# Kernel optimization log

Hardware: AMD Instinct MI355X
Metric: run time of the kernel (lower is better)

## Reference

```python
import jax, jax.numpy as jnp
import numpy as np

N_NODES = 100000
N_EDGES = 1600000
D_IN = 64
D_OUT = 64
NEG_SLOPE = 0.2


def setup_inputs() -> dict:
    key = jax.random.key(0)
    ks = jax.random.split(key, 10)
    x = jax.random.normal(ks[0], (N_NODES, D_IN), dtype=jnp.float32)
    edge_index = jax.random.randint(ks[1], (2, N_EDGES), 0, N_NODES, dtype=jnp.int64)
    # glorot-ish scales
    s_lin = 1.0 / np.sqrt(D_IN)
    W_lin = jax.random.normal(ks[2], (D_IN, D_OUT), dtype=jnp.float32) * s_lin
    att_src = jax.random.normal(ks[3], (D_OUT,), dtype=jnp.float32) * s_lin
    att_dst = jax.random.normal(ks[4], (D_OUT,), dtype=jnp.float32) * s_lin
    bias = jnp.zeros((D_OUT,), dtype=jnp.float32)
    W1 = jax.random.normal(ks[5], (D_IN, D_OUT // 2), dtype=jnp.float32) * s_lin
    b1 = jnp.zeros((D_OUT // 2,), dtype=jnp.float32)
    W2 = jax.random.normal(ks[6], (D_OUT // 2, 1), dtype=jnp.float32) * (1.0 / np.sqrt(D_OUT // 2))
    b2 = jnp.zeros((1,), dtype=jnp.float32)
    return {"x": x, "edge_index": edge_index, "W_lin": W_lin, "att_src": att_src,
            "att_dst": att_dst, "bias": bias, "W1": W1, "b1": b1, "W2": W2, "b2": b2}


def reference(x, edge_index, W_lin, att_src, att_dst, bias, W1, b1, W2, b2):
    N = x.shape[0]
    h = x @ W_lin  # [N, D_OUT]
    # peak detector applied to projected features (module requires in==out)
    peak = jax.nn.sigmoid(jax.nn.gelu(h @ W1 + b1, approximate=False) @ W2 + b2)  # [N,1]
    row, col = edge_index[0], edge_index[1]
    # (cat(src,dst) * att).sum(-1) == (h@att_src)[row] + (h@att_dst)[col]
    a_s = h @ att_src  # [N]
    a_d = h @ att_dst  # [N]
    alpha = a_s[row] + a_d[col]  # [E]
    alpha = jnp.where(alpha >= 0, alpha, NEG_SLOPE * alpha)  # leaky_relu
    # segment softmax keyed on row
    m = jax.ops.segment_max(alpha, row, num_segments=N)  # [N]
    e = jnp.exp(alpha - m[row])
    s = jax.ops.segment_sum(e, row, num_segments=N)  # [N]
    alpha = e / s[row]
    # scatter-add weighted source messages back to row (dropout=identity in eval)
    out = jax.ops.segment_sum(h[row] * alpha[:, None], row, num_segments=N)  # [N, D_OUT]
    out = out * (1.0 + peak) + bias
    return out
```

## Files before the change

### kernel.cpp

```cpp
#include <hip/hip_runtime.h>
#include <math.h>

#define D 64
#define DH 32

typedef __attribute__((ext_vector_type(8))) short bf16x8;
typedef __attribute__((ext_vector_type(4))) float f32x4;

static __device__ __forceinline__ unsigned short f2b(float f) {
    unsigned int u = __builtin_bit_cast(unsigned int, f);
    u += 0x7FFFu + ((u >> 16) & 1u);
    return (unsigned short)(u >> 16);
}
static __device__ __forceinline__ unsigned int pack_b2(float a, float b) {
    return (unsigned int)f2b(a) | ((unsigned int)f2b(b) << 16);
}
static __device__ __forceinline__ float gelu_fast(float v) {
    const float ax = fabsf(v) * 0.70710678118654752f;
    const float t  = __builtin_amdgcn_rcpf(fmaf(0.3275911f, ax, 1.0f));
    float poly = fmaf(1.061405429f, t, -1.453152027f);
    poly = fmaf(poly, t, 1.421413741f);
    poly = fmaf(poly, t, -0.284496736f);
    poly = fmaf(poly, t, 0.254829592f);
    poly *= t;
    float er = fmaf(-poly, __expf(-ax * ax), 1.0f);
    er = copysignf(er, v);
    return 0.5f * v * (1.0f + er);
}

__global__ void edge_flag_kernel(const int* __restrict__ row,
                                 unsigned char* __restrict__ flag, int E) {
    int i4 = (blockIdx.x * blockDim.x + threadIdx.x) * 4;
    if (i4 + 3 < E) {
        int4 r = *(const int4*)(row + i4);
        flag[r.x] = 1; flag[r.y] = 1; flag[r.z] = 1; flag[r.w] = 1;
    } else if (i4 < E) {
        for (int j = i4; j < E; ++j) flag[row[j]] = 1;
    }
}

__global__ void prep_kernel(const float* __restrict__ Wlin, const float* __restrict__ W1,
                            const float* __restrict__ bias, const float* __restrict__ b1,
                            const float* __restrict__ W2,
                            uint4* __restrict__ flag4, int nflag4,
                            unsigned short* __restrict__ packAW,
                            unsigned short* __restrict__ packAW1, float* __restrict__ packBias,
                            float* __restrict__ packB1, float* __restrict__ packW2)
{
    const int idx = blockIdx.x * blockDim.x + threadIdx.x;
    const int stride = gridDim.x * blockDim.x;
    const uint4 z = {0u, 0u, 0u, 0u};
    for (int i = idx; i < nflag4; i += stride) flag4[i] = z;

    if (blockIdx.x == 0) {
        const int lane = threadIdx.x & 63, part = threadIdx.x >> 6;
        const int q = lane >> 4, m = lane & 15;
#pragma unroll
        for (int fo = 0; fo < 2; ++fo) {
            const int f = part * 2 + fo, nt = f >> 1, ks = f & 1;
#pragma unroll
            for (int j = 0; j < 8; ++j) {
                const int k = 32 * ks + 8 * q + j, n = 16 * nt + m;
                packAW[(f * 64 + lane) * 8 + j] = f2b(Wlin[k * D + n]);
            }
        }
        {
            const int f = part, ntW = f >> 1, ks = f & 1;
#pragma unroll
            for (int j = 0; j < 8; ++j) {
                const int k = 32 * ks + 8 * q + j, n = 16 * ntW + m;
                packAW1[(f * 64 + lane) * 8 + j] = f2b(W1[k * DH + n]);
            }
        }
#pragma unroll
        for (int r = 0; r < 4; ++r)
            packBias[(part * 64 + lane) * 4 + r] = bias[16 * part + 4 * q + r];
        if (part < 2) {
#pragma unroll
            for (int r = 0; r < 4; ++r)
                packB1[(part * 64 + lane) * 4 + r] = b1[16 * part + 4 * q + r];
        } else {
#pragma unroll
            for (int r = 0; r < 4; ++r)
                packW2[((part - 2) * 64 + lane) * 4 + r] = W2[16 * (part - 2) + 4 * q + r];
        }
    }
}

__global__ __launch_bounds__(256) void gat_mfma5(
    const float* __restrict__ x, const unsigned char* __restrict__ flag,
    const unsigned short* __restrict__ packAW, const unsigned short* __restrict__ packAW1,
    const float* __restrict__ packBias, const float* __restrict__ packB1,
    const float* __restrict__ packW2, const float* __restrict__ b2,
    float* __restrict__ out, int N, int ntiles)
{
    __shared__ unsigned short sH[4][16][72];

    const int tid  = threadIdx.x;
    const int wv   = tid >> 6;
    const int lane = tid & 63;
    const int q    = lane >> 4;
    const int m    = lane & 15;

    bf16x8 aw[4][2], aw1[2][2];
#pragma unroll
    for (int nt = 0; nt < 4; ++nt)
#pragma unroll
        for (int ks = 0; ks < 2; ++ks)
            aw[nt][ks] = ((const bf16x8*)packAW)[(nt * 2 + ks) * 64 + lane];
#pragma unroll
    for (int nt = 0; nt < 2; ++nt)
#pragma unroll
        for (int ks = 0; ks < 2; ++ks)
            aw1[nt][ks] = ((const bf16x8*)packAW1)[(nt * 2 + ks) * 64 + lane];
    const f32x4 b1v0 = ((const f32x4*)packB1)[0 * 64 + lane];
    const f32x4 b1v1 = ((const f32x4*)packB1)[1 * 64 + lane];
    const f32x4 w2v0 = ((const f32x4*)packW2)[0 * 64 + lane];
    const f32x4 w2v1 = ((const f32x4*)packW2)[1 * 64 + lane];
    f32x4 biasv[4];
#pragma unroll
    for (int nt = 0; nt < 4; ++nt) biasv[nt] = ((const f32x4*)packBias)[nt * 64 + lane];
    const float b2s = b2[0];

    int t = blockIdx.x;
    if (t >= ntiles) return;

    float4 cu0, cu1, cu2, cu3; unsigned char cfl;
    {
        int g = t * 64 + wv * 16 + m; if (g > N - 1) g = N - 1;
        const float* px = x + (size_t)g * D + 8 * q;
        cu0 = *(const float4*)(px);      cu1 = *(const float4*)(px + 4);
        cu2 = *(const float4*)(px + 32); cu3 = *(const float4*)(px + 36);
        cfl = flag[g];
    }

    while (true) {
        const int tn = t + gridDim.x;
        const bool more = tn < ntiles;
        float4 nu0, nu1, nu2, nu3; unsigned char nfl = 0;
        if (more) {
            int g = tn * 64 + wv * 16 + m; if (g > N - 1) g = N - 1;
            const float* px = x + (size_t)g * D + 8 * q;
            nu0 = *(const float4*)(px);      nu1 = *(const float4*)(px + 4);
            nu2 = *(const float4*)(px + 32); nu3 = *(const float4*)(px + 36);
            nfl = flag[g];
        }

        uint4 pk0, pk1;
        pk0.x = pack_b2(cu0.x, cu0.y); pk0.y = pack_b2(cu0.z, cu0.w);
        pk0.z = pack_b2(cu1.x, cu1.y); pk0.w = pack_b2(cu1.z, cu1.w);
        pk1.x = pack_b2(cu2.x, cu2.y); pk1.y = pack_b2(cu2.z, cu2.w);
        pk1.z = pack_b2(cu3.x, cu3.y); pk1.w = pack_b2(cu3.z, cu3.w);
        const bf16x8 bx0 = __builtin_bit_cast(bf16x8, pk0);
        const bf16x8 bx1 = __builtin_bit_cast(bf16x8, pk1);

        f32x4 accH[4];
#pragma unroll
        for (int nt = 0; nt < 4; ++nt) accH[nt] = (f32x4){0.f, 0.f, 0.f, 0.f};
#pragma unroll
        for (int nt = 0; nt < 4; ++nt)
            accH[nt] = __builtin_amdgcn_mfma_f32_16x16x32_bf16(aw[nt][0], bx0, accH[nt], 0, 0, 0);
#pragma unroll
        for (int nt = 0; nt < 4; ++nt)
            accH[nt] = __builtin_amdgcn_mfma_f32_16x16x32_bf16(aw[nt][1], bx1, accH[nt], 0, 0, 0);

        asm volatile("" ::: "memory");
#pragma unroll
        for (int nt = 0; nt < 4; ++nt) {
            uint2 pk;
            pk.x = pack_b2(accH[nt][0], accH[nt][1]);
            pk.y = pack_b2(accH[nt][2], accH[nt][3]);
            *(uint2*)&sH[wv][m][16 * nt + 4 * q] = pk;
        }
        asm volatile("" ::: "memory");
        const bf16x8 a20 = *(const bf16x8*)&sH[wv][m][8 * q];
        const bf16x8 a21 = *(const bf16x8*)&sH[wv][m][32 + 8 * q];

        f32x4 acc20 = b1v0, acc21 = b1v1;
        acc20 = __builtin_amdgcn_mfma_f32_16x16x32_bf16(aw1[0][0], a20, acc20, 0, 0, 0);
        acc20 = __builtin_amdgcn_mfma_f32_16x16x32_bf16(aw1[0][1], a21, acc20, 0, 0, 0);
        acc21 = __builtin_amdgcn_mfma_f32_16x16x32_bf16(aw1[1][0], a20, acc21, 0, 0, 0);
        acc21 = __builtin_amdgcn_mfma_f32_16x16x32_bf16(aw1[1][1], a21, acc21, 0, 0, 0);

        float pp = 0.f;
#pragma unroll
        for (int r = 0; r < 4; ++r) {
            pp = fmaf(gelu_fast(acc20[r]), w2v0[r], pp);
            pp = fmaf(gelu_fast(acc21[r]), w2v1[r], pp);
        }
        pp += __shfl_xor(pp, 16);
        pp += __shfl_xor(pp, 32);
        const float sg = __builtin_amdgcn_rcpf(1.f + __expf(-(pp + b2s)));
        const float scale = (cfl != 0) ? (1.f + sg) : 0.f;

        const int g = t * 64 + wv * 16 + m;
        if (g < N) {
            float* po = out + (size_t)g * D + 4 * q;
#pragma unroll
            for (int nt = 0; nt < 4; ++nt) {
                f32x4 o;
#pragma unroll
                for (int r = 0; r < 4; ++r)
                    o[r] = fmaf(accH[nt][r], scale, biasv[nt][r]);
                *(f32x4*)(po + 16 * nt) = o;
            }
        }

        if (!more) break;
        cu0 = nu0; cu1 = nu1; cu2 = nu2; cu3 = nu3; cfl = nfl;
        t = tn;
    }
}

extern "C" void kernel_launch(void* const* d_in, const int* in_sizes, int n_in,
                              void* d_out, int out_size, void* d_ws, size_t ws_size,
                              hipStream_t stream) {
    const float* x    = (const float*)d_in[0];
    const int*   eidx = (const int*)d_in[1];
    const float* Wlin = (const float*)d_in[2];
    const float* bias = (const float*)d_in[5];
    const float* W1   = (const float*)d_in[6];
    const float* b1   = (const float*)d_in[7];
    const float* W2   = (const float*)d_in[8];
    const float* b2   = (const float*)d_in[9];
    float* out = (float*)d_out;

    const int N = in_sizes[0] / D;
    const int E = in_sizes[1] / 2;

    char* ws = (char*)d_ws;
    unsigned char* flag = (unsigned char*)ws;
    const int nflag4 = (N + 15) / 16;
    const size_t off = (((size_t)nflag4 * 16) + 255) & ~(size_t)255;
    unsigned short* packAW   = (unsigned short*)(ws + off);
    unsigned short* packAW1  = (unsigned short*)(ws + off + 8192);
    float*          packBias = (float*)(ws + off + 12288);
    float*          packB1   = (float*)(ws + off + 16384);
    float*          packW2   = (float*)(ws + off + 18432);

    const int ntiles  = (N + 63) / 64;
    const int nblocks = (ntiles < 512) ? ntiles : 512;

    prep_kernel<<<256, 256, 0, stream>>>(Wlin, W1, bias, b1, W2,
                                         (uint4*)flag, nflag4,
                                         packAW, packAW1, packBias, packB1, packW2);
    edge_flag_kernel<<<(E / 4 + 255) / 256, 256, 0, stream>>>(eidx, flag, E);
    gat_mfma5<<<nblocks, 256, 0, stream>>>(x, flag, packAW, packAW1,
                                           packBias, packB1, packW2, b2, out, N, ntiles);
}
```

Before: 31.55 us.

## Drop prep kernel: pack weights in-kernel, memset flags, widen edge flagging

Removes the separate prep kernel. The main kernel now converts Wlin/W1 to bf16 fragments and loads the bias vectors directly from the raw inputs, and the flag array is cleared with hipMemsetAsync. The edge-flag kernel now handles 8 edges per thread instead of 4. The aim is to save a kernel launch and its serialization cost. In exchange, every block repeats strided scalar weight loads and conversions in its prologue.

```diff
diff --git a/kernel.cpp b/kernel.cpp
--- a/kernel.cpp
+++ b/kernel.cpp
@@ -30,68 +30,22 @@
 
 __global__ void edge_flag_kernel(const int* __restrict__ row,
                                  unsigned char* __restrict__ flag, int E) {
-    int i4 = (blockIdx.x * blockDim.x + threadIdx.x) * 4;
-    if (i4 + 3 < E) {
-        int4 r = *(const int4*)(row + i4);
-        flag[r.x] = 1; flag[r.y] = 1; flag[r.z] = 1; flag[r.w] = 1;
-    } else if (i4 < E) {
-        for (int j = i4; j < E; ++j) flag[row[j]] = 1;
-    }
-}
-
-__global__ void prep_kernel(const float* __restrict__ Wlin, const float* __restrict__ W1,
-                            const float* __restrict__ bias, const float* __restrict__ b1,
-                            const float* __restrict__ W2,
-                            uint4* __restrict__ flag4, int nflag4,
-                            unsigned short* __restrict__ packAW,
-                            unsigned short* __restrict__ packAW1, float* __restrict__ packBias,
-                            float* __restrict__ packB1, float* __restrict__ packW2)
-{
-    const int idx = blockIdx.x * blockDim.x + threadIdx.x;
-    const int stride = gridDim.x * blockDim.x;
-    const uint4 z = {0u, 0u, 0u, 0u};
-    for (int i = idx; i < nflag4; i += stride) flag4[i] = z;
-
-    if (blockIdx.x == 0) {
-        const int lane = threadIdx.x & 63, part = threadIdx.x >> 6;
-        const int q = lane >> 4, m = lane & 15;
-#pragma unroll
-        for (int fo = 0; fo < 2; ++fo) {
-            const int f = part * 2 + fo, nt = f >> 1, ks = f & 1;
-#pragma unroll
-            for (int j = 0; j < 8; ++j) {
-                const int k = 32 * ks + 8 * q + j, n = 16 * nt + m;
-                packAW[(f * 64 + lane) * 8 + j] = f2b(Wlin[k * D + n]);
-            }
-        }
-        {
-            const int f = part, ntW = f >> 1, ks = f & 1;
-#pragma unroll
-            for (int j = 0; j < 8; ++j) {
-                const int k = 32 * ks + 8 * q + j, n = 16 * ntW + m;
-                packAW1[(f * 64 + lane) * 8 + j] = f2b(W1[k * DH + n]);
-            }
-        }
-#pragma unroll
-        for (int r = 0; r < 4; ++r)
-            packBias[(part * 64 + lane) * 4 + r] = bias[16 * part + 4 * q + r];
-        if (part < 2) {
-#pragma unroll
-            for (int r = 0; r < 4; ++r)
-                packB1[(part * 64 + lane) * 4 + r] = b1[16 * part + 4 * q + r];
-        } else {
-#pragma unroll
-            for (int r = 0; r < 4; ++r)
-                packW2[((part - 2) * 64 + lane) * 4 + r] = W2[16 * (part - 2) + 4 * q + r];
-        }
-    }
-}
-
-__global__ __launch_bounds__(256) void gat_mfma5(
+    const int base = (blockIdx.x * blockDim.x + threadIdx.x) * 8;
+    if (base + 7 < E) {
+        const int4 a = *(const int4*)(row + base);
+        const int4 b = *(const int4*)(row + base + 4);
+        flag[a.x] = 1; flag[a.y] = 1; flag[a.z] = 1; flag[a.w] = 1;
+        flag[b.x] = 1; flag[b.y] = 1; flag[b.z] = 1; flag[b.w] = 1;
+    } else if (base < E) {
+        for (int j = base; j < E; ++j) flag[row[j]] = 1;
+    }
+}
+
+__global__ __launch_bounds__(256) void gat_mfma6(
     const float* __restrict__ x, const unsigned char* __restrict__ flag,
-    const unsigned short* __restrict__ packAW, const unsigned short* __restrict__ packAW1,
-    const float* __restrict__ packBias, const float* __restrict__ packB1,
-    const float* __restrict__ packW2, const float* __restrict__ b2,
+    const float* __restrict__ Wlin, const float* __restrict__ bias,
+    const float* __restrict__ W1, const float* __restrict__ b1,
+    const float* __restrict__ W2, const float* __restrict__ b2,
     float* __restrict__ out, int N, int ntiles)
 {
     __shared__ unsigned short sH[4][16][72];
@@ -106,20 +60,35 @@
 #pragma unroll
     for (int nt = 0; nt < 4; ++nt)
 #pragma unroll
-        for (int ks = 0; ks < 2; ++ks)
-            aw[nt][ks] = ((const bf16x8*)packAW)[(nt * 2 + ks) * 64 + lane];
+        for (int ks = 0; ks < 2; ++ks) {
+            bf16x8 a;
+#pragma unroll
+            for (int j = 0; j < 8; ++j)
+                a[j] = (short)f2b(Wlin[(32 * ks + 8 * q + j) * D + 16 * nt + m]);
+            aw[nt][ks] = a;
+        }
 #pragma unroll
     for (int nt = 0; nt < 2; ++nt)
 #pragma unroll
-        for (int ks = 0; ks < 2; ++ks)
-            aw1[nt][ks] = ((const bf16x8*)packAW1)[(nt * 2 + ks) * 64 + lane];
-    const f32x4 b1v0 = ((const f32x4*)packB1)[0 * 64 + lane];
-    const f32x4 b1v1 = ((const f32x4*)packB1)[1 * 64 + lane];
-    const f32x4 w2v0 = ((const f32x4*)packW2)[0 * 64 + lane];
-    const f32x4 w2v1 = ((const f32x4*)packW2)[1 * 64 + lane];
+        for (int ks = 0; ks < 2; ++ks) {
+            bf16x8 a;
+#pragma unroll
+            for (int j = 0; j < 8; ++j)
+                a[j] = (short)f2b(W1[(32 * ks + 8 * q + j) * DH + 16 * nt + m]);
+            aw1[nt][ks] = a;
+        }
+    f32x4 b1v0, b1v1, w2v0, w2v1;
     f32x4 biasv[4];
 #pragma unroll
-    for (int nt = 0; nt < 4; ++nt) biasv[nt] = ((const f32x4*)packBias)[nt * 64 + lane];
+    for (int r = 0; r < 4; ++r) {
+        b1v0[r] = b1[4 * q + r];
+        b1v1[r] = b1[16 + 4 * q + r];
+        w2v0[r] = W2[4 * q + r];
+        w2v1[r] = W2[16 + 4 * q + r];
+#pragma unroll
+        for (int nt = 0; nt < 4; ++nt)
+            biasv[nt][r] = bias[16 * nt + 4 * q + r];
+    }
     const float b2s = b2[0];
 
     int t = blockIdx.x;
@@ -228,23 +197,13 @@
     const int N = in_sizes[0] / D;
     const int E = in_sizes[1] / 2;
 
-    char* ws = (char*)d_ws;
-    unsigned char* flag = (unsigned char*)ws;
-    const int nflag4 = (N + 15) / 16;
-    const size_t off = (((size_t)nflag4 * 16) + 255) & ~(size_t)255;
-    unsigned short* packAW   = (unsigned short*)(ws + off);
-    unsigned short* packAW1  = (unsigned short*)(ws + off + 8192);
-    float*          packBias = (float*)(ws + off + 12288);
-    float*          packB1   = (float*)(ws + off + 16384);
-    float*          packW2   = (float*)(ws + off + 18432);
+    unsigned char* flag = (unsigned char*)d_ws;
 
     const int ntiles  = (N + 63) / 64;
     const int nblocks = (ntiles < 512) ? ntiles : 512;
 
-    prep_kernel<<<256, 256, 0, stream>>>(Wlin, W1, bias, b1, W2,
-                                         (uint4*)flag, nflag4,
-                                         packAW, packAW1, packBias, packB1, packW2);
-    edge_flag_kernel<<<(E / 4 + 255) / 256, 256, 0, stream>>>(eidx, flag, E);
-    gat_mfma5<<<nblocks, 256, 0, stream>>>(x, flag, packAW, packAW1,
-                                           packBias, packB1, packW2, b2, out, N, ntiles);
-}
+    hipMemsetAsync(flag, 0, (size_t)N, stream);
+    edge_flag_kernel<<<(E / 8 + 255) / 256, 256, 0, stream>>>(eidx, flag, E);
+    gat_mfma6<<<nblocks, 256, 0, stream>>>(x, flag, Wlin, bias, W1, b1, W2, b2,
+                                           out, N, ntiles);
+}
```

New measurement: 32.43 us. +2.8%, slower.

## Switch main kernel to single-wave blocks and widen edge-flag per-thread work

Applied to the files above, without the earlier changes.

The fused projection/peak kernel now runs one wave per block, with each block handling a 16-row group, and a larger persistent grid of 3072 blocks in place of 512 four-wave blocks. This is meant to spread work more finely across CUs and improve latency hiding with smaller shared-memory footprints. The edge-flag kernel now has each thread process 8 row indices instead of 4, halving its grid. The trade-off is more per-block setup, since each block reloads the packed weights.

```diff
diff --git a/kernel.cpp b/kernel.cpp
--- a/kernel.cpp
+++ b/kernel.cpp
@@ -30,12 +30,14 @@
 
 __global__ void edge_flag_kernel(const int* __restrict__ row,
                                  unsigned char* __restrict__ flag, int E) {
-    int i4 = (blockIdx.x * blockDim.x + threadIdx.x) * 4;
-    if (i4 + 3 < E) {
-        int4 r = *(const int4*)(row + i4);
-        flag[r.x] = 1; flag[r.y] = 1; flag[r.z] = 1; flag[r.w] = 1;
-    } else if (i4 < E) {
-        for (int j = i4; j < E; ++j) flag[row[j]] = 1;
+    const int base = (blockIdx.x * blockDim.x + threadIdx.x) * 8;
+    if (base + 7 < E) {
+        const int4 a = *(const int4*)(row + base);
+        const int4 b = *(const int4*)(row + base + 4);
+        flag[a.x] = 1; flag[a.y] = 1; flag[a.z] = 1; flag[a.w] = 1;
+        flag[b.x] = 1; flag[b.y] = 1; flag[b.z] = 1; flag[b.w] = 1;
+    } else if (base < E) {
+        for (int j = base; j < E; ++j) flag[row[j]] = 1;
     }
 }
 
@@ -59,18 +61,14 @@
         for (int fo = 0; fo < 2; ++fo) {
             const int f = part * 2 + fo, nt = f >> 1, ks = f & 1;
 #pragma unroll
-            for (int j = 0; j < 8; ++j) {
-                const int k = 32 * ks + 8 * q + j, n = 16 * nt + m;
-                packAW[(f * 64 + lane) * 8 + j] = f2b(Wlin[k * D + n]);
-            }
+            for (int j = 0; j < 8; ++j)
+                packAW[(f * 64 + lane) * 8 + j] = f2b(Wlin[(32 * ks + 8 * q + j) * D + 16 * nt + m]);
         }
         {
             const int f = part, ntW = f >> 1, ks = f & 1;
 #pragma unroll
-            for (int j = 0; j < 8; ++j) {
-                const int k = 32 * ks + 8 * q + j, n = 16 * ntW + m;
-                packAW1[(f * 64 + lane) * 8 + j] = f2b(W1[k * DH + n]);
-            }
+            for (int j = 0; j < 8; ++j)
+                packAW1[(f * 64 + lane) * 8 + j] = f2b(W1[(32 * ks + 8 * q + j) * DH + 16 * ntW + m]);
         }
 #pragma unroll
         for (int r = 0; r < 4; ++r)
@@ -87,18 +85,16 @@
     }
 }
 
-__global__ __launch_bounds__(256) void gat_mfma5(
+__global__ __launch_bounds__(64, 4) void gat_mfma8(
     const float* __restrict__ x, const unsigned char* __restrict__ flag,
     const unsigned short* __restrict__ packAW, const unsigned short* __restrict__ packAW1,
     const float* __restrict__ packBias, const float* __restrict__ packB1,
     const float* __restrict__ packW2, const float* __restrict__ b2,
-    float* __restrict__ out, int N, int ntiles)
+    float* __restrict__ out, int N, int ngroups)
 {
-    __shared__ unsigned short sH[4][16][72];
-
-    const int tid  = threadIdx.x;
-    const int wv   = tid >> 6;
-    const int lane = tid & 63;
+    __shared__ unsigned short sH[16][72];
+
+    const int lane = threadIdx.x & 63;
     const int q    = lane >> 4;
     const int m    = lane & 15;
 
@@ -122,12 +118,12 @@
     for (int nt = 0; nt < 4; ++nt) biasv[nt] = ((const f32x4*)packBias)[nt * 64 + lane];
     const float b2s = b2[0];
 
-    int t = blockIdx.x;
-    if (t >= ntiles) return;
+    int gi = blockIdx.x;
+    if (gi >= ngroups) return;
 
     float4 cu0, cu1, cu2, cu3; unsigned char cfl;
     {
-        int g = t * 64 + wv * 16 + m; if (g > N - 1) g = N - 1;
+        int g = gi * 16 + m; if (g > N - 1) g = N - 1;
         const float* px = x + (size_t)g * D + 8 * q;
         cu0 = *(const float4*)(px);      cu1 = *(const float4*)(px + 4);
         cu2 = *(const float4*)(px + 32); cu3 = *(const float4*)(px + 36);
@@ -135,11 +131,11 @@
     }
 
     while (true) {
-        const int tn = t + gridDim.x;
-        const bool more = tn < ntiles;
+        const int gin = gi + gridDim.x;
+        const bool more = gin < ngroups;
         float4 nu0, nu1, nu2, nu3; unsigned char nfl = 0;
         if (more) {
-            int g = tn * 64 + wv * 16 + m; if (g > N - 1) g = N - 1;
+            int g = gin * 16 + m; if (g > N - 1) g = N - 1;
             const float* px = x + (size_t)g * D + 8 * q;
             nu0 = *(const float4*)(px);      nu1 = *(const float4*)(px + 4);
             nu2 = *(const float4*)(px + 32); nu3 = *(const float4*)(px + 36);
@@ -170,11 +166,11 @@
             uint2 pk;
             pk.x = pack_b2(accH[nt][0], accH[nt][1]);
             pk.y = pack_b2(accH[nt][2], accH[nt][3]);
-            *(uint2*)&sH[wv][m][16 * nt + 4 * q] = pk;
+            *(uint2*)&sH[m][16 * nt + 4 * q] = pk;
         }
         asm volatile("" ::: "memory");
-        const bf16x8 a20 = *(const bf16x8*)&sH[wv][m][8 * q];
-        const bf16x8 a21 = *(const bf16x8*)&sH[wv][m][32 + 8 * q];
+        const bf16x8 a20 = *(const bf16x8*)&sH[m][8 * q];
+        const bf16x8 a21 = *(const bf16x8*)&sH[m][32 + 8 * q];
 
         f32x4 acc20 = b1v0, acc21 = b1v1;
         acc20 = __builtin_amdgcn_mfma_f32_16x16x32_bf16(aw1[0][0], a20, acc20, 0, 0, 0);
@@ -193,7 +189,7 @@
         const float sg = __builtin_amdgcn_rcpf(1.f + __expf(-(pp + b2s)));
         const float scale = (cfl != 0) ? (1.f + sg) : 0.f;
 
-        const int g = t * 64 + wv * 16 + m;
+        const int g = gi * 16 + m;
         if (g < N) {
             float* po = out + (size_t)g * D + 4 * q;
 #pragma unroll
@@ -208,7 +204,7 @@
 
         if (!more) break;
         cu0 = nu0; cu1 = nu1; cu2 = nu2; cu3 = nu3; cfl = nfl;
-        t = tn;
+        gi = gin;
     }
 }
 
@@ -238,13 +234,13 @@
     float*          packB1   = (float*)(ws + off + 16384);
     float*          packW2   = (float*)(ws + off + 18432);
 
-    const int ntiles  = (N + 63) / 64;
-    const int nblocks = (ntiles < 512) ? ntiles : 512;
+    const int ngroups = (N + 15) / 16;
+    const int nblocks = (ngroups < 3072) ? ngroups : 3072;
 
     prep_kernel<<<256, 256, 0, stream>>>(Wlin, W1, bias, b1, W2,
                                          (uint4*)flag, nflag4,
                                          packAW, packAW1, packBias, packB1, packW2);
-    edge_flag_kernel<<<(E / 4 + 255) / 256, 256, 0, stream>>>(eidx, flag, E);
-    gat_mfma5<<<nblocks, 256, 0, stream>>>(x, flag, packAW, packAW1,
-                                           packBias, packB1, packW2, b2, out, N, ntiles);
-}
+    edge_flag_kernel<<<(E / 8 + 255) / 256, 256, 0, stream>>>(eidx, flag, E);
+    gat_mfma8<<<nblocks, 64, 0, stream>>>(x, flag, packAW, packAW1,
+                                          packBias, packB1, packW2, b2, out, N, ngroups);
+}
```

After: 37.59 us. 1.19x slower.
